# Optimization experiments

Measured on AMD Instinct MI355X. Metric: run time of the kernel, lower is better.

## Reference

```python
import jax, jax.numpy as jnp
import numpy as np

NUM_CLASSES = 20
NUM_ANCHORS = 3
STRIDES = (8, 16, 32)
FMP = (320, 160, 80)
TOPK = 100
CONF_THRESH = 0.01
NMS_THRESH = 0.5
ANCHOR_SIZE = np.array([[12, 16], [19, 36], [40, 28], [36, 75], [76, 55], [72, 146],
                        [142, 110], [192, 243], [459, 401]], dtype=np.float32).reshape(3, NUM_ANCHORS, 2)


def make_anchors(level):
    h = w = FMP[level]
    ys, xs = jnp.meshgrid(jnp.arange(h, dtype=jnp.float32), jnp.arange(w, dtype=jnp.float32), indexing='ij')
    xy = jnp.stack([xs, ys], axis=-1).reshape(-1, 1, 2) + 0.5            # [HW,1,2] grid centers
    xy = jnp.broadcast_to(xy, (h * w, NUM_ANCHORS, 2))
    wh = jnp.broadcast_to(jnp.asarray(ANCHOR_SIZE[level]), (h * w, NUM_ANCHORS, 2))
    return jnp.concatenate([xy, wh], axis=-1).reshape(-1, 4)             # [HW*A, 4]


def level_topk(obj, cls, reg, level):
    C = NUM_CLASSES
    # [1, ch, H, W] -> [H*W*A, ch_per_anchor], matching permute(1,2,0).view(-1, .)
    obj = obj[0].transpose(1, 2, 0).reshape(-1, 1)
    cls = cls[0].transpose(1, 2, 0).reshape(-1, C)
    reg = reg[0].transpose(1, 2, 0).reshape(-1, 4)
    anchors = make_anchors(level)
    # decode: ctr = (sigmoid(txy)*3 - 1.5 + grid) * stride ; wh = exp(twh) * anchor_wh
    ctr = (jax.nn.sigmoid(reg[:, :2]) * 3.0 - 1.5 + anchors[:, :2]) * STRIDES[level]
    wh = jnp.exp(reg[:, 2:]) * anchors[:, 2:]
    boxes = jnp.concatenate([ctr - 0.5 * wh, ctr + 0.5 * wh], axis=-1)   # [N, 4] xyxy
    scores = (jax.nn.sigmoid(obj) * jax.nn.sigmoid(cls)).reshape(-1)     # [N*C]
    top_s, top_i = jax.lax.top_k(scores, TOPK)
    anchor_idx = top_i // C
    labels = top_i % C
    return top_s, labels, boxes[anchor_idx], top_s > CONF_THRESH


def nms_fixed(boxes, scores, labels, valid):
    # class-aware greedy NMS on a fixed candidate set; suppressed entries get score 0 / keep False
    K = scores.shape[0]
    order = jnp.argsort(-scores)
    b, s, l, v = boxes[order], scores[order], labels[order], valid[order]
    areas = (b[:, 2] - b[:, 0]) * (b[:, 3] - b[:, 1])
    xx1 = jnp.maximum(b[:, None, 0], b[None, :, 0])
    yy1 = jnp.maximum(b[:, None, 1], b[None, :, 1])
    xx2 = jnp.minimum(b[:, None, 2], b[None, :, 2])
    yy2 = jnp.minimum(b[:, None, 3], b[None, :, 3])
    inter = jnp.maximum(1e-10, xx2 - xx1) * jnp.maximum(1e-10, yy2 - yy1)
    iou = inter / (areas[:, None] + areas[None, :] - inter)
    sup_mat = (iou > NMS_THRESH) & (l[:, None] == l[None, :])            # per-class suppression
    idx = jnp.arange(K)

    def body(i, state):
        suppressed, keep = state
        is_kept = jnp.logical_and(jnp.logical_not(suppressed[i]), v[i])
        keep = keep.at[i].set(is_kept)
        suppressed = suppressed | (is_kept & sup_mat[i] & (idx > i))
        return suppressed, keep

    _, keep = jax.lax.fori_loop(0, K, body, (jnp.zeros(K, bool), jnp.zeros(K, bool)))
    return b, s * keep.astype(s.dtype), l, keep


def setup_inputs() -> dict:
    key = jax.random.key(0)
    ks = jax.random.split(key, 9)
    shapes = {
        'obj0': (1, NUM_ANCHORS, 320, 320), 'cls0': (1, NUM_ANCHORS * NUM_CLASSES, 320, 320), 'reg0': (1, NUM_ANCHORS * 4, 320, 320),
        'obj1': (1, NUM_ANCHORS, 160, 160), 'cls1': (1, NUM_ANCHORS * NUM_CLASSES, 160, 160), 'reg1': (1, NUM_ANCHORS * 4, 160, 160),
        'obj2': (1, NUM_ANCHORS, 80, 80), 'cls2': (1, NUM_ANCHORS * NUM_CLASSES, 80, 80), 'reg2': (1, NUM_ANCHORS * 4, 80, 80),
    }
    return {name: jax.random.normal(k, shp, dtype=jnp.float32)
            for k, (name, shp) in zip(ks, shapes.items())}


def reference(obj0, cls0, reg0, obj1, cls1, reg1, obj2, cls2, reg2):
    levels = [(obj0, cls0, reg0), (obj1, cls1, reg1), (obj2, cls2, reg2)]
    parts = [level_topk(o, c, r, i) for i, (o, c, r) in enumerate(levels)]
    scores = jnp.concatenate([p[0] for p in parts])
    labels = jnp.concatenate([p[1] for p in parts])
    boxes = jnp.concatenate([p[2] for p in parts])
    valid = jnp.concatenate([p[3] for p in parts])
    return nms_fixed(boxes, scores, labels, valid)  # (bboxes[300,4], scores[300], labels[300], keep[300])
```

## Files before the change

kernel.cpp:

```cpp
#include <hip/hip_runtime.h>
#include <stdint.h>

typedef unsigned int u32;
typedef unsigned long long u64;

#define TOPK 100
#define CAP 4096
#define NB 512
#define BINBASE 32000u
#define KAB_BLOCKS 788

__device__ const float ANC[3][3][2] = {
  {{12.f,16.f},{19.f,36.f},{40.f,28.f}},
  {{36.f,75.f},{76.f,55.f},{72.f,146.f}},
  {{142.f,110.f},{192.f,243.f},{459.f,401.f}}
};

__device__ __forceinline__ float sigmoidf_(float x) {
  if (x >= 0.f) return 1.f / (1.f + expf(-x));
  float e = expf(x);
  return e / (1.f + e);
}

__device__ __forceinline__ float fcomp2(const float2& v, int q) {
  return q ? v.y : v.x;
}

__global__ __launch_bounds__(256) void kA_scan(
    const float* __restrict__ obj0, const float* __restrict__ cls0,
    const float* __restrict__ obj1, const float* __restrict__ cls1,
    const float* __restrict__ obj2, const float* __restrict__ cls2,
    u32* __restrict__ hist, float* __restrict__ amax)
{
  __shared__ u32 h[NB];
  int tid = threadIdx.x;
  h[tid] = 0; h[tid + 256] = 0;
  __syncthreads();

  int b = blockIdx.x;
  const float *obj, *cls; int P, L, abase; u32 task;
  if (b < 600)      { L=0; obj=obj0; cls=cls0; P=102400; abase=0;      task=(u32)(b*256+tid); }
  else if (b < 750) { L=1; obj=obj1; cls=cls1; P=25600;  abase=307200; task=(u32)((b-600)*256+tid); }
  else              { L=2; obj=obj2; cls=cls2; P=6400;   abase=384000; task=(u32)((b-750)*256+tid); }
  int tpa = P >> 1;
  bool valid = task < (u32)(3*tpa);

  if (valid) {
    int a = (int)(task / (u32)tpa), rem = (int)(task % (u32)tpa);
    int p0 = rem * 2;
    float2 o2 = *(const float2*)(obj + a*P + p0);
    const float* cp = cls + (size_t)(a*20)*P + p0;
    float2 cv[20];
    #pragma unroll
    for (int k = 0; k < 20; ++k) cv[k] = *(const float2*)(cp + (size_t)k*P);
    float2 cm = cv[0];
    #pragma unroll
    for (int k = 1; k < 20; ++k) {
      cm.x = fmaxf(cm.x, cv[k].x); cm.y = fmaxf(cm.y, cv[k].y);
    }
    float2 am2;
    am2.x = sigmoidf_(o2.x) * sigmoidf_(cm.x);
    am2.y = sigmoidf_(o2.y) * sigmoidf_(cm.y);
    *(float2*)(amax + abase + a*P + p0) = am2;
    #pragma unroll
    for (int q = 0; q < 2; ++q) {
      u32 bt = __float_as_uint(fcomp2(am2, q));
      if (bt >= (BINBASE << 15)) {
        u32 bin = (bt >> 15) - BINBASE;
        if (bin < NB) atomicAdd(&h[bin], 1u);
      }
    }
  }
  __syncthreads();
  if (h[tid])       atomicAdd(&hist[L*NB + tid],       h[tid]);
  if (h[tid + 256]) atomicAdd(&hist[L*NB + tid + 256], h[tid + 256]);
}

__global__ __launch_bounds__(256) void kB_collect(
    const float* __restrict__ obj0, const float* __restrict__ cls0,
    const float* __restrict__ obj1, const float* __restrict__ cls1,
    const float* __restrict__ obj2, const float* __restrict__ cls2,
    const float* __restrict__ amax, const u32* __restrict__ hist,
    u32* __restrict__ cnt, u64* __restrict__ cand)
{
  __shared__ u32 s[NB];
  __shared__ u32 sThr;
  int tid = threadIdx.x;
  int b = blockIdx.x;
  const float *obj, *cls; int P, L, abase; u32 task;
  if (b < 600)      { L=0; obj=obj0; cls=cls0; P=102400; abase=0;      task=(u32)(b*256+tid); }
  else if (b < 750) { L=1; obj=obj1; cls=cls1; P=25600;  abase=307200; task=(u32)((b-600)*256+tid); }
  else              { L=2; obj=obj2; cls=cls2; P=6400;   abase=384000; task=(u32)((b-750)*256+tid); }
  int tpa = P >> 1;
  bool valid = task < (u32)(3*tpa);

  s[tid] = hist[L*NB + tid]; s[tid + 256] = hist[L*NB + tid + 256];
  __syncthreads();
  for (int off = 1; off < NB; off <<= 1) {
    u32 v0 = s[tid]       + ((tid + off < NB)       ? s[tid + off]       : 0u);
    u32 v1 = s[tid + 256] + ((tid + 256 + off < NB) ? s[tid + 256 + off] : 0u);
    __syncthreads();
    s[tid] = v0; s[tid + 256] = v1;
    __syncthreads();
  }
  if (tid == 0 && s[0] < TOPK) sThr = BINBASE << 15;
  {
    int i0 = tid, i1 = tid + 256;
    u32 a0 = s[i0], n0 = (i0 + 1 < NB) ? s[i0 + 1] : 0u;
    if (a0 >= TOPK && n0 < TOPK) sThr = (BINBASE + (u32)i0) << 15;
    u32 a1 = s[i1], n1 = (i1 + 1 < NB) ? s[i1 + 1] : 0u;
    if (a1 >= TOPK && n1 < TOPK) sThr = (BINBASE + (u32)i1) << 15;
  }
  __syncthreads();
  u32 thr = sThr;

  if (valid) {
    int a = (int)(task / (u32)tpa), rem = (int)(task % (u32)tpa);
    int p0 = rem * 2;
    float2 am2 = *(const float2*)(amax + abase + a*P + p0);
    bool any = (__float_as_uint(am2.x) >= thr) | (__float_as_uint(am2.y) >= thr);
    if (any) {
      float2 o2 = *(const float2*)(obj + a*P + p0);
      const float* cp = cls + (size_t)(a*20)*P + p0;
      float2 cv[20];
      #pragma unroll
      for (int k = 0; k < 20; ++k) cv[k] = *(const float2*)(cp + (size_t)k*P);
      #pragma unroll
      for (int q = 0; q < 2; ++q) {
        if (__float_as_uint(fcomp2(am2, q)) >= thr) {
          float so = sigmoidf_(fcomp2(o2, q));
          int p = p0 + q;
          #pragma unroll
          for (int k = 0; k < 20; ++k) {
            float sc = so * sigmoidf_(fcomp2(cv[k], q));
            u32 bits = __float_as_uint(sc);
            if (bits >= thr) {
              u32 pos = atomicAdd(&cnt[L], 1u);
              u32 idx = (u32)(p*60 + a*20 + k);
              if (pos < CAP) cand[L*CAP + pos] = ((u64)bits << 32) | (u64)(0x00FFFFFFu - idx);
            }
          }
        }
      }
    }
  }
}

__global__ __launch_bounds__(1024) void kT_select_nms(
    const float* __restrict__ reg0, const float* __restrict__ reg1, const float* __restrict__ reg2,
    const u64* __restrict__ cand, const u32* __restrict__ cnt,
    u64* __restrict__ matg, u32* __restrict__ bar,
    float* __restrict__ out)
{
  extern __shared__ uint8_t smem[];
  u64*    mat   = (u64*)(smem);
  float4* ibox4 = (float4*)(smem + 12000);
  float2* iml2  = (float2*)(smem + 16800);
  float*  x1s   = (float*)(smem + 19200);
  float*  y1s   = (float*)(smem + 20400);
  float*  x2s   = (float*)(smem + 21600);
  float*  y2s   = (float*)(smem + 22800);
  float*  sc2   = (float*)(smem + 24000);
  int*    lb2   = (int*)(smem + 25200);
  int*    vd2   = (int*)(smem + 26400);
  u64*    rowAny= (u64*)(smem + 27600);
  u64*    km    = (u64*)(smem + 27648);
  float*  ars   = (float*)(smem + 27696);
  u64*    sel   = (u64*)(smem + 28896);

  int tid = threadIdx.x;
  int b = blockIdx.x;
  if (tid < 300) sel[tid] = 0ull;
  __syncthreads();

  {
    int gL    = (tid >= 768) ? 2 : (tid >= 384) ? 1 : 0;
    int gbase = (gL == 2) ? 768 : (gL == 1) ? 384 : 0;
    int lt    = tid - gbase;
    int gsz   = (gL == 2) ? 256 : 384;

    u32 n = cnt[gL]; if (n > CAP) n = CAP;
    bool useLds = (n <= 496);
    u64* kc = mat + gL*500;
    const u64* cb = cand + gL*CAP;
    u32 n4 = (n + 3u) & ~3u;

    if (useLds) {
      for (u32 j = (u32)lt; j < n; j += gsz) kc[j] = cb[j];
      if (lt < 4 && n + (u32)lt < n4) kc[n + lt] = 0ull;
    }
    __syncthreads();

    if (useLds) {
      for (u32 j = (u32)lt; j < n; j += gsz) {
        u64 kk = kc[j]; int r = 0;
        for (u32 t = 0; t < n4; t += 4) {
          u64 k0 = kc[t], k1 = kc[t+1], k2 = kc[t+2], k3 = kc[t+3];
          r += (k0 > kk) ? 1 : 0; r += (k1 > kk) ? 1 : 0;
          r += (k2 > kk) ? 1 : 0; r += (k3 > kk) ? 1 : 0;
        }
        if (r < TOPK) sel[gL*TOPK + r] = kk;
      }
    } else {
      u32 nn = n & ~3u;
      for (u32 j = (u32)lt; j < n; j += gsz) {
        u64 kk = cb[j]; int r = 0;
        for (u32 t = 0; t < nn; t += 4) {
          r += (cb[t]   > kk) ? 1 : 0; r += (cb[t+1] > kk) ? 1 : 0;
          r += (cb[t+2] > kk) ? 1 : 0; r += (cb[t+3] > kk) ? 1 : 0;
        }
        for (u32 t = nn; t < n; ++t) r += (cb[t] > kk) ? 1 : 0;
        if (r < TOPK) sel[gL*TOPK + r] = kk;
      }
    }
  }
  __syncthreads();

  if (tid < 300) {
    int Lm = tid / TOPK, rr = tid % TOPK;
    u64 key = sel[tid];

    const float* reg; int Pq, W, stride;
    if (Lm == 0)      { reg = reg0; Pq = 102400; W = 320; stride = 8; }
    else if (Lm == 1) { reg = reg1; Pq = 25600;  W = 160; stride = 16; }
    else              { reg = reg2; Pq = 6400;   W = 80;  stride = 32; }
    float x1, y1, x2, y2, score; int lab, vld;
    if (key == 0) {
      x1 = y1 = x2 = y2 = 0.f; score = 0.f; lab = 0; vld = 0;
    } else {
      score = __uint_as_float((u32)(key >> 32));
      u32 i = 0x00FFFFFFu - (u32)(key & 0xFFFFFFFFull);
      int c = (int)(i % 60u), p = (int)(i / 60u);
      int aa = c / 20, k = c % 20;
      int x = p % W, y = p / W;
      float tx = reg[(aa*4+0)*Pq + p], ty = reg[(aa*4+1)*Pq + p];
      float tw = reg[(aa*4+2)*Pq + p], th = reg[(aa*4+3)*Pq + p];
      float cx = (sigmoidf_(tx)*3.f - 1.5f + (float)x + 0.5f) * (float)stride;
      float cy = (sigmoidf_(ty)*3.f - 1.5f + (float)y + 0.5f) * (float)stride;
      float bw = expf(tw) * ANC[Lm][aa][0];
      float bh = expf(th) * ANC[Lm][aa][1];
      lab = k; vld = (score > 0.01f) ? 1 : 0;
      x1 = cx - 0.5f*bw; y1 = cy - 0.5f*bh;
      x2 = cx + 0.5f*bw; y2 = cy + 0.5f*bh;
    }

    int rank = rr;
    #pragma unroll
    for (int Lo = 0; Lo < 3; ++Lo) {
      if (Lo == Lm) continue;
      const u64* arr = sel + Lo*TOPK;
      bool ge = (Lo < Lm);
      int lo = 0;
      #pragma unroll
      for (int st = 64; st > 0; st >>= 1) {
        int nxt = lo + st;
        if (nxt <= TOPK) {
          u64 v = arr[nxt - 1];
          bool pred = ge ? (v >= key) : (v > key);
          if (pred) lo = nxt;
        }
      }
      rank += lo;
    }

    float ar = (x2 - x1) * (y2 - y1);
    ibox4[rank] = make_float4(x1, y1, x2, y2);
    iml2[rank]  = make_float2(ar, (float)lab);
    x1s[rank] = x1; y1s[rank] = y1; x2s[rank] = x2; y2s[rank] = y2; ars[rank] = ar;
    sc2[rank] = score; lb2[rank] = lab; vd2[rank] = vld;
  }
  __syncthreads();

  {
    int w = (b == 0) ? 4 : (b - 1);
    int wave = tid >> 6, lane = tid & 63;
    int j = w*64 + lane;
    bool jv = j < 300;
    float jx1=0.f, jy1=0.f, jx2=0.f, jy2=0.f, jar=0.f; float jlb=-1.f;
    if (jv) { jx1=x1s[j]; jy1=y1s[j]; jx2=x2s[j]; jy2=y2s[j]; jar=ars[j]; jlb=(float)lb2[j]; }
    int ilim = (w+1)*64; if (ilim > 300) ilim = 300;
    for (int i = wave; i < ilim; i += 16) {
      float4 B = ibox4[i];
      float2 M = iml2[i];
      float xx1 = fmaxf(B.x, jx1), yy1 = fmaxf(B.y, jy1);
      float xx2 = fminf(B.z, jx2), yy2 = fminf(B.w, jy2);
      float inter = fmaxf(1e-10f, xx2-xx1) * fmaxf(1e-10f, yy2-yy1);
      float iou = inter / (M.x + jar - inter);
      bool pred = jv && (iou > 0.5f) && (M.y == jlb);
      u64 m = __ballot(pred);
      if (lane == 0) {
        if (b == 0) mat[i*5 + 4] = m;
        else __hip_atomic_store(&matg[i*5 + w], m, __ATOMIC_RELAXED, __HIP_MEMORY_SCOPE_AGENT);
      }
    }
  }
  __syncthreads();

  if (b != 0) {
    if (tid == 0)
      __hip_atomic_fetch_add(bar, 1u, __ATOMIC_RELEASE, __HIP_MEMORY_SCOPE_AGENT);
    return;
  }

  if (tid == 0) {
    while (__hip_atomic_load(bar, __ATOMIC_ACQUIRE, __HIP_MEMORY_SCOPE_AGENT) < 4u)
      __builtin_amdgcn_s_sleep(1);
  }
  __syncthreads();
  for (int idx = tid; idx < 1200; idx += 1024) {
    int w2 = idx / 300, i = idx % 300;
    if (i < (w2+1)*64)
      mat[i*5 + w2] = __hip_atomic_load(&matg[i*5 + w2], __ATOMIC_RELAXED, __HIP_MEMORY_SCOPE_AGENT);
  }
  __syncthreads();

  {
    bool flag = false;
    if (tid < 300) {
      int c = tid >> 6, bq = tid & 63;
      u64 acc = mat[tid*5 + c] & ((bq == 63) ? 0ull : (~0ull << (bq + 1)));
      for (int w = c + 1; w < 5; ++w) acc |= mat[tid*5 + w];
      flag = (acc != 0ull);
    }
    u64 bal = __ballot(flag);
    if ((tid & 63) == 0 && (tid >> 6) < 5) rowAny[tid >> 6] = bal;
  }
  __syncthreads();

  if (tid < 64) {
    int lane = tid;
    u64 vm[5];
    #pragma unroll
    for (int c = 0; c < 5; ++c) {
      int j = c*64 + lane;
      vm[c] = __ballot((j < 300) && (vd2[j] != 0));
    }
    u64 ra[5];
    #pragma unroll
    for (int c = 0; c < 5; ++c) ra[c] = rowAny[c];
    u64 S[5] = {0,0,0,0,0};
    #pragma unroll
    for (int c = 0; c < 5; ++c) {
      u64 kbits = 0;
      int lim = (c == 4) ? 44 : 64;
      for (int t = 0; t < lim; ++t) {
        u64 kept = ((~(S[c] >> t)) & (vm[c] >> t)) & 1ull;
        kbits |= kept << t;
        if (kept & ((ra[c] >> t) & 1ull)) {
          int i = c*64 + t;
          #pragma unroll
          for (int w = 0; w < 5; ++w)
            if (w >= c) S[w] |= mat[i*5 + w];
        }
      }
      if (lane == 0) km[c] = kbits;
    }
  }
  __syncthreads();

  if (tid < 300) {
    float kf = (float)((km[tid >> 6] >> (tid & 63)) & 1ull);
    float4 bq = ibox4[tid];
    out[tid*4+0] = bq.x; out[tid*4+1] = bq.y;
    out[tid*4+2] = bq.z; out[tid*4+3] = bq.w;
    out[1200+tid] = sc2[tid] * kf;
    out[1500+tid] = (float)lb2[tid];
    out[1800+tid] = kf;
  }
}

extern "C" void kernel_launch(void* const* d_in, const int* in_sizes, int n_in,
                              void* d_out, int out_size, void* d_ws, size_t ws_size,
                              hipStream_t stream) {
  const float* obj0 = (const float*)d_in[0];
  const float* cls0 = (const float*)d_in[1];
  const float* reg0 = (const float*)d_in[2];
  const float* obj1 = (const float*)d_in[3];
  const float* cls1 = (const float*)d_in[4];
  const float* reg1 = (const float*)d_in[5];
  const float* obj2 = (const float*)d_in[6];
  const float* cls2 = (const float*)d_in[7];
  const float* reg2 = (const float*)d_in[8];
  float* out = (float*)d_out;

  uint8_t* ws = (uint8_t*)d_ws;
  u32*   hist = (u32*)(ws + 0);
  u32*   cnt  = (u32*)(ws + 6144);
  u32*   bar  = (u32*)(ws + 6156);
  u64*   cand = (u64*)(ws + 8192);
  u64*   matg = (u64*)(ws + 106496);
  float* amax = (float*)(ws + 118496);

  (void)hipMemsetAsync(ws, 0, 6160, stream);

  kA_scan<<<dim3(KAB_BLOCKS), dim3(256), 0, stream>>>(
      obj0, cls0, obj1, cls1, obj2, cls2, hist, amax);
  kB_collect<<<dim3(KAB_BLOCKS), dim3(256), 0, stream>>>(
      obj0, cls0, obj1, cls1, obj2, cls2, amax, hist, cnt, cand);
  kT_select_nms<<<dim3(5), dim3(1024), 31296, stream>>>(
      reg0, reg1, reg2, cand, cnt, matg, bar, out);
}
```

Measured before the change: 145.2 us.

## Fuse collect and NMS kernels using a device-wide completion counter

Merges the candidate-collection kernel and the select/NMS kernel into one launch. Blocks 0-4 spin on a global done counter until all 788 collect blocks have finished, then do the top-k selection and NMS with 256 threads instead of 1024. This removes one kernel launch and the gap between launches. In exchange, the NMS stage gets a quarter of the threads, and it relies on all collect blocks being scheduled while the five waiting blocks hold their CUs, which risks deadlock or delay. Every collect block now allocates 31KB of LDS, which may lower its occupancy.

```diff
diff --git a/kernel.cpp b/kernel.cpp
--- a/kernel.cpp
+++ b/kernel.cpp
@@ -8,7 +8,9 @@
 #define CAP 4096
 #define NB 512
 #define BINBASE 32000u
-#define KAB_BLOCKS 788
+#define KA_BLOCKS 788
+#define NCOLLECT 788
+#define KBT_BLOCKS 793
 
 __device__ const float ANC[3][3][2] = {
   {{12.f,16.f},{19.f,36.f},{40.f,28.f}},
@@ -76,83 +78,90 @@
   if (h[tid + 256]) atomicAdd(&hist[L*NB + tid + 256], h[tid + 256]);
 }
 
-__global__ __launch_bounds__(256) void kB_collect(
+__global__ __launch_bounds__(256) void kBT2_collect_nms(
     const float* __restrict__ obj0, const float* __restrict__ cls0,
     const float* __restrict__ obj1, const float* __restrict__ cls1,
     const float* __restrict__ obj2, const float* __restrict__ cls2,
+    const float* __restrict__ reg0, const float* __restrict__ reg1, const float* __restrict__ reg2,
     const float* __restrict__ amax, const u32* __restrict__ hist,
-    u32* __restrict__ cnt, u64* __restrict__ cand)
+    u32* __restrict__ cnt, u64* __restrict__ cand,
+    u32* __restrict__ done, u32* __restrict__ bar, u64* __restrict__ matg,
+    float* __restrict__ out)
 {
-  __shared__ u32 s[NB];
-  __shared__ u32 sThr;
+  extern __shared__ uint8_t smem[];
   int tid = threadIdx.x;
   int b = blockIdx.x;
-  const float *obj, *cls; int P, L, abase; u32 task;
-  if (b < 600)      { L=0; obj=obj0; cls=cls0; P=102400; abase=0;      task=(u32)(b*256+tid); }
-  else if (b < 750) { L=1; obj=obj1; cls=cls1; P=25600;  abase=307200; task=(u32)((b-600)*256+tid); }
-  else              { L=2; obj=obj2; cls=cls2; P=6400;   abase=384000; task=(u32)((b-750)*256+tid); }
-  int tpa = P >> 1;
-  bool valid = task < (u32)(3*tpa);
-
-  s[tid] = hist[L*NB + tid]; s[tid + 256] = hist[L*NB + tid + 256];
-  __syncthreads();
-  for (int off = 1; off < NB; off <<= 1) {
-    u32 v0 = s[tid]       + ((tid + off < NB)       ? s[tid + off]       : 0u);
-    u32 v1 = s[tid + 256] + ((tid + 256 + off < NB) ? s[tid + 256 + off] : 0u);
+
+  if (b >= 5) {
+    u32* s = (u32*)smem;
+    u32* sThrP = (u32*)(smem + 2048);
+    int cb = b - 5;
+    const float *obj, *cls; int P, L, abase; u32 task;
+    if (cb < 600)      { L=0; obj=obj0; cls=cls0; P=102400; abase=0;      task=(u32)(cb*256+tid); }
+    else if (cb < 750) { L=1; obj=obj1; cls=cls1; P=25600;  abase=307200; task=(u32)((cb-600)*256+tid); }
+    else               { L=2; obj=obj2; cls=cls2; P=6400;   abase=384000; task=(u32)((cb-750)*256+tid); }
+    int tpa = P >> 1;
+    bool valid = task < (u32)(3*tpa);
+
+    s[tid] = hist[L*NB + tid]; s[tid + 256] = hist[L*NB + tid + 256];
     __syncthreads();
-    s[tid] = v0; s[tid + 256] = v1;
+    for (int off = 1; off < NB; off <<= 1) {
+      u32 v0 = s[tid]       + ((tid + off < NB)       ? s[tid + off]       : 0u);
+      u32 v1 = s[tid + 256] + ((tid + 256 + off < NB) ? s[tid + 256 + off] : 0u);
+      __syncthreads();
+      s[tid] = v0; s[tid + 256] = v1;
+      __syncthreads();
+    }
+    if (tid == 0 && s[0] < TOPK) *sThrP = BINBASE << 15;
+    {
+      int i0 = tid, i1 = tid + 256;
+      u32 a0 = s[i0], n0 = (i0 + 1 < NB) ? s[i0 + 1] : 0u;
+      if (a0 >= TOPK && n0 < TOPK) *sThrP = (BINBASE + (u32)i0) << 15;
+      u32 a1 = s[i1], n1 = (i1 + 1 < NB) ? s[i1 + 1] : 0u;
+      if (a1 >= TOPK && n1 < TOPK) *sThrP = (BINBASE + (u32)i1) << 15;
+    }
     __syncthreads();
-  }
-  if (tid == 0 && s[0] < TOPK) sThr = BINBASE << 15;
-  {
-    int i0 = tid, i1 = tid + 256;
-    u32 a0 = s[i0], n0 = (i0 + 1 < NB) ? s[i0 + 1] : 0u;
-    if (a0 >= TOPK && n0 < TOPK) sThr = (BINBASE + (u32)i0) << 15;
-    u32 a1 = s[i1], n1 = (i1 + 1 < NB) ? s[i1 + 1] : 0u;
-    if (a1 >= TOPK && n1 < TOPK) sThr = (BINBASE + (u32)i1) << 15;
-  }
-  __syncthreads();
-  u32 thr = sThr;
-
-  if (valid) {
-    int a = (int)(task / (u32)tpa), rem = (int)(task % (u32)tpa);
-    int p0 = rem * 2;
-    float2 am2 = *(const float2*)(amax + abase + a*P + p0);
-    bool any = (__float_as_uint(am2.x) >= thr) | (__float_as_uint(am2.y) >= thr);
-    if (any) {
-      float2 o2 = *(const float2*)(obj + a*P + p0);
-      const float* cp = cls + (size_t)(a*20)*P + p0;
-      float2 cv[20];
-      #pragma unroll
-      for (int k = 0; k < 20; ++k) cv[k] = *(const float2*)(cp + (size_t)k*P);
-      #pragma unroll
-      for (int q = 0; q < 2; ++q) {
-        if (__float_as_uint(fcomp2(am2, q)) >= thr) {
-          float so = sigmoidf_(fcomp2(o2, q));
-          int p = p0 + q;
-          #pragma unroll
-          for (int k = 0; k < 20; ++k) {
-            float sc = so * sigmoidf_(fcomp2(cv[k], q));
-            u32 bits = __float_as_uint(sc);
-            if (bits >= thr) {
-              u32 pos = atomicAdd(&cnt[L], 1u);
-              u32 idx = (u32)(p*60 + a*20 + k);
-              if (pos < CAP) cand[L*CAP + pos] = ((u64)bits << 32) | (u64)(0x00FFFFFFu - idx);
+    u32 thr = *sThrP;
+
+    if (valid) {
+      int a = (int)(task / (u32)tpa), rem = (int)(task % (u32)tpa);
+      int p0 = rem * 2;
+      float2 am2 = *(const float2*)(amax + abase + a*P + p0);
+      bool any = (__float_as_uint(am2.x) >= thr) | (__float_as_uint(am2.y) >= thr);
+      if (any) {
+        float2 o2 = *(const float2*)(obj + a*P + p0);
+        const float* cp = cls + (size_t)(a*20)*P + p0;
+        float2 cv[20];
+        #pragma unroll
+        for (int k = 0; k < 20; ++k) cv[k] = *(const float2*)(cp + (size_t)k*P);
+        #pragma unroll
+        for (int q = 0; q < 2; ++q) {
+          if (__float_as_uint(fcomp2(am2, q)) >= thr) {
+            float so = sigmoidf_(fcomp2(o2, q));
+            int p = p0 + q;
+            #pragma unroll
+            for (int k = 0; k < 20; ++k) {
+              float sc = so * sigmoidf_(fcomp2(cv[k], q));
+              u32 bits = __float_as_uint(sc);
+              if (bits >= thr) {
+                u32 pos = atomicAdd(&cnt[L], 1u);
+                u32 idx = (u32)(p*60 + a*20 + k);
+                if (pos < CAP)
+                  __hip_atomic_store(&cand[L*CAP + pos],
+                                     ((u64)bits << 32) | (u64)(0x00FFFFFFu - idx),
+                                     __ATOMIC_RELAXED, __HIP_MEMORY_SCOPE_AGENT);
+              }
             }
           }
         }
       }
     }
-  }
-}
-
-__global__ __launch_bounds__(1024) void kT_select_nms(
-    const float* __restrict__ reg0, const float* __restrict__ reg1, const float* __restrict__ reg2,
-    const u64* __restrict__ cand, const u32* __restrict__ cnt,
-    u64* __restrict__ matg, u32* __restrict__ bar,
-    float* __restrict__ out)
-{
-  extern __shared__ uint8_t smem[];
+    __syncthreads();
+    if (tid == 0)
+      __hip_atomic_fetch_add(done, 1u, __ATOMIC_RELEASE, __HIP_MEMORY_SCOPE_AGENT);
+    return;
+  }
+
   u64*    mat   = (u64*)(smem);
   float4* ibox4 = (float4*)(smem + 12000);
   float2* iml2  = (float2*)(smem + 16800);
@@ -168,25 +177,33 @@
   float*  ars   = (float*)(smem + 27696);
   u64*    sel   = (u64*)(smem + 28896);
 
-  int tid = threadIdx.x;
-  int b = blockIdx.x;
-  if (tid < 300) sel[tid] = 0ull;
+  int role = b;
+
+  if (tid == 0) {
+    while (__hip_atomic_load(done, __ATOMIC_ACQUIRE, __HIP_MEMORY_SCOPE_AGENT) < (u32)NCOLLECT)
+      __builtin_amdgcn_s_sleep(2);
+  }
+  __syncthreads();
+
+  for (int t0 = tid; t0 < 300; t0 += 256) sel[t0] = 0ull;
   __syncthreads();
 
   {
-    int gL    = (tid >= 768) ? 2 : (tid >= 384) ? 1 : 0;
-    int gbase = (gL == 2) ? 768 : (gL == 1) ? 384 : 0;
+    int gL    = (tid >= 192) ? 2 : (tid >= 96) ? 1 : 0;
+    int gbase = (gL == 2) ? 192 : (gL == 1) ? 96 : 0;
     int lt    = tid - gbase;
-    int gsz   = (gL == 2) ? 256 : 384;
-
-    u32 n = cnt[gL]; if (n > CAP) n = CAP;
+    int gsz   = (gL == 2) ? 64 : 96;
+
+    u32 n = __hip_atomic_load(&cnt[gL], __ATOMIC_RELAXED, __HIP_MEMORY_SCOPE_AGENT);
+    if (n > CAP) n = CAP;
     bool useLds = (n <= 496);
     u64* kc = mat + gL*500;
-    const u64* cb = cand + gL*CAP;
+    const u64* cb2 = cand + gL*CAP;
     u32 n4 = (n + 3u) & ~3u;
 
     if (useLds) {
-      for (u32 j = (u32)lt; j < n; j += gsz) kc[j] = cb[j];
+      for (u32 j = (u32)lt; j < n; j += gsz)
+        kc[j] = __hip_atomic_load(&cb2[j], __ATOMIC_RELAXED, __HIP_MEMORY_SCOPE_AGENT);
       if (lt < 4 && n + (u32)lt < n4) kc[n + lt] = 0ull;
     }
     __syncthreads();
@@ -202,23 +219,20 @@
         if (r < TOPK) sel[gL*TOPK + r] = kk;
       }
     } else {
-      u32 nn = n & ~3u;
       for (u32 j = (u32)lt; j < n; j += gsz) {
-        u64 kk = cb[j]; int r = 0;
-        for (u32 t = 0; t < nn; t += 4) {
-          r += (cb[t]   > kk) ? 1 : 0; r += (cb[t+1] > kk) ? 1 : 0;
-          r += (cb[t+2] > kk) ? 1 : 0; r += (cb[t+3] > kk) ? 1 : 0;
-        }
-        for (u32 t = nn; t < n; ++t) r += (cb[t] > kk) ? 1 : 0;
+        u64 kk = __hip_atomic_load(&cb2[j], __ATOMIC_RELAXED, __HIP_MEMORY_SCOPE_AGENT);
+        int r = 0;
+        for (u32 t = 0; t < n; ++t)
+          r += (__hip_atomic_load(&cb2[t], __ATOMIC_RELAXED, __HIP_MEMORY_SCOPE_AGENT) > kk) ? 1 : 0;
         if (r < TOPK) sel[gL*TOPK + r] = kk;
       }
     }
   }
   __syncthreads();
 
-  if (tid < 300) {
-    int Lm = tid / TOPK, rr = tid % TOPK;
-    u64 key = sel[tid];
+  for (int t0 = tid; t0 < 300; t0 += 256) {
+    int Lm = t0 / TOPK, rr = t0 % TOPK;
+    u64 key = sel[t0];
 
     const float* reg; int Pq, W, stride;
     if (Lm == 0)      { reg = reg0; Pq = 102400; W = 320; stride = 8; }
@@ -272,14 +286,14 @@
   __syncthreads();
 
   {
-    int w = (b == 0) ? 4 : (b - 1);
+    int w = (role == 0) ? 4 : (role - 1);
     int wave = tid >> 6, lane = tid & 63;
     int j = w*64 + lane;
     bool jv = j < 300;
     float jx1=0.f, jy1=0.f, jx2=0.f, jy2=0.f, jar=0.f; float jlb=-1.f;
     if (jv) { jx1=x1s[j]; jy1=y1s[j]; jx2=x2s[j]; jy2=y2s[j]; jar=ars[j]; jlb=(float)lb2[j]; }
     int ilim = (w+1)*64; if (ilim > 300) ilim = 300;
-    for (int i = wave; i < ilim; i += 16) {
+    for (int i = wave; i < ilim; i += 4) {
       float4 B = ibox4[i];
       float2 M = iml2[i];
       float xx1 = fmaxf(B.x, jx1), yy1 = fmaxf(B.y, jy1);
@@ -289,14 +303,14 @@
       bool pred = jv && (iou > 0.5f) && (M.y == jlb);
       u64 m = __ballot(pred);
       if (lane == 0) {
-        if (b == 0) mat[i*5 + 4] = m;
+        if (role == 0) mat[i*5 + 4] = m;
         else __hip_atomic_store(&matg[i*5 + w], m, __ATOMIC_RELAXED, __HIP_MEMORY_SCOPE_AGENT);
       }
     }
   }
   __syncthreads();
 
-  if (b != 0) {
+  if (role != 0) {
     if (tid == 0)
       __hip_atomic_fetch_add(bar, 1u, __ATOMIC_RELEASE, __HIP_MEMORY_SCOPE_AGENT);
     return;
@@ -307,7 +321,7 @@
       __builtin_amdgcn_s_sleep(1);
   }
   __syncthreads();
-  for (int idx = tid; idx < 1200; idx += 1024) {
+  for (int idx = tid; idx < 1200; idx += 256) {
     int w2 = idx / 300, i = idx % 300;
     if (i < (w2+1)*64)
       mat[i*5 + w2] = __hip_atomic_load(&matg[i*5 + w2], __ATOMIC_RELAXED, __HIP_MEMORY_SCOPE_AGENT);
@@ -316,14 +330,25 @@
 
   {
     bool flag = false;
-    if (tid < 300) {
-      int c = tid >> 6, bq = tid & 63;
-      u64 acc = mat[tid*5 + c] & ((bq == 63) ? 0ull : (~0ull << (bq + 1)));
-      for (int w = c + 1; w < 5; ++w) acc |= mat[tid*5 + w];
+    {
+      int row = tid, c = row >> 6, bq = row & 63;
+      u64 acc = mat[row*5 + c] & ((bq == 63) ? 0ull : (~0ull << (bq + 1)));
+      for (int w = c + 1; w < 5; ++w) acc |= mat[row*5 + w];
       flag = (acc != 0ull);
     }
     u64 bal = __ballot(flag);
-    if ((tid & 63) == 0 && (tid >> 6) < 5) rowAny[tid >> 6] = bal;
+    if ((tid & 63) == 0) rowAny[tid >> 6] = bal;
+    bool flag2 = false;
+    {
+      int row = 256 + tid;
+      if (row < 300) {
+        int bq = row & 63;
+        u64 acc = mat[row*5 + 4] & ((bq == 63) ? 0ull : (~0ull << (bq + 1)));
+        flag2 = (acc != 0ull);
+      }
+    }
+    u64 bal2 = __ballot(flag2);
+    if (tid == 0) rowAny[4] = bal2;
   }
   __syncthreads();
 
@@ -358,14 +383,14 @@
   }
   __syncthreads();
 
-  if (tid < 300) {
-    float kf = (float)((km[tid >> 6] >> (tid & 63)) & 1ull);
-    float4 bq = ibox4[tid];
-    out[tid*4+0] = bq.x; out[tid*4+1] = bq.y;
-    out[tid*4+2] = bq.z; out[tid*4+3] = bq.w;
-    out[1200+tid] = sc2[tid] * kf;
-    out[1500+tid] = (float)lb2[tid];
-    out[1800+tid] = kf;
+  for (int t0 = tid; t0 < 300; t0 += 256) {
+    float kf = (float)((km[t0 >> 6] >> (t0 & 63)) & 1ull);
+    float4 bq = ibox4[t0];
+    out[t0*4+0] = bq.x; out[t0*4+1] = bq.y;
+    out[t0*4+2] = bq.z; out[t0*4+3] = bq.w;
+    out[1200+t0] = sc2[t0] * kf;
+    out[1500+t0] = (float)lb2[t0];
+    out[1800+t0] = kf;
   }
 }
 
@@ -387,16 +412,16 @@
   u32*   hist = (u32*)(ws + 0);
   u32*   cnt  = (u32*)(ws + 6144);
   u32*   bar  = (u32*)(ws + 6156);
+  u32*   done = (u32*)(ws + 6160);
   u64*   cand = (u64*)(ws + 8192);
   u64*   matg = (u64*)(ws + 106496);
   float* amax = (float*)(ws + 118496);
 
-  (void)hipMemsetAsync(ws, 0, 6160, stream);
-
-  kA_scan<<<dim3(KAB_BLOCKS), dim3(256), 0, stream>>>(
+  (void)hipMemsetAsync(ws, 0, 6164, stream);
+
+  kA_scan<<<dim3(KA_BLOCKS), dim3(256), 0, stream>>>(
       obj0, cls0, obj1, cls1, obj2, cls2, hist, amax);
-  kB_collect<<<dim3(KAB_BLOCKS), dim3(256), 0, stream>>>(
-      obj0, cls0, obj1, cls1, obj2, cls2, amax, hist, cnt, cand);
-  kT_select_nms<<<dim3(5), dim3(1024), 31296, stream>>>(
-      reg0, reg1, reg2, cand, cnt, matg, bar, out);
+  kBT2_collect_nms<<<dim3(KBT_BLOCKS), dim3(256), 31296, stream>>>(
+      obj0, cls0, obj1, cls1, obj2, cls2, reg0, reg1, reg2,
+      amax, hist, cnt, cand, done, bar, matg, out);
 }
```

Result: slower. 171.3 us (+18.0%).
